# Kernel tuning notes

Measured on AMD Instinct MI355X. Metric: run time of the kernel, lower is better.

Reference implementation:

```python
import jax, jax.numpy as jnp
import numpy as np

STATE_MASS = 4.0
EPS = 1e-5
LOW_RANK_SCALE = 0.1  # _LOW_RANK_SCALE_INIT


def _ln(x, g, b):
    mu = jnp.mean(x, axis=-1, keepdims=True)
    var = jnp.var(x, axis=-1, keepdims=True)
    return (x - mu) * jax.lax.rsqrt(var + EPS) * g + b


def _signed_abs_softmax(s, axis=-1):
    s = jnp.nan_to_num(s)
    return jnp.sign(s) * jax.nn.softmax(jnp.abs(s), axis=axis)


def _signed_softmax_state(st):
    st = jnp.nan_to_num(st)
    return jnp.sign(st) * jax.nn.softmax(jnp.abs(st), axis=-1) * STATE_MASS


def _low_rank_scores(dst, src, Ut_w, Ut_b, Us_w, Us_b, w):
    # bilinear low-rank pairwise: score[b,i,j] = sum_r (dst_i Ut)_r * w_r * (src_j Us)_r
    pt = dst @ Ut_w + Ut_b                      # [B,Nd,R]
    ps = src @ Us_w + Us_b                      # [B,Ns,R]
    return jnp.einsum('bir,r,bjr->bij', pt, w * LOW_RANK_SCALE, ps)


def _gather_rows(x, idx):
    # x: [B,N,...], idx: [B,M,K] -> [B,M,K,...] (per-batch gather, no NxM broadcast)
    return jax.vmap(lambda xi, ii: xi[ii])(x, idx)


def setup_inputs() -> dict:
    key = jax.random.key(0)
    ks = jax.random.split(key, 8)
    B, S, D, M, R = 16, 2048, 512, 256, 64
    std = 0.02
    return {
        'token_val': jax.random.normal(ks[0], (B, S, D), jnp.float32),
        'token_state': jax.random.normal(ks[1], (B, S), jnp.float32),
        'init_state': jax.random.normal(ks[2], (M,), jnp.float32) * std,
        'init_val': jax.random.normal(ks[3], (M, D), jnp.float32) * std,
        'rUs_w': jax.random.normal(ks[4], (D, R), jnp.float32) * std,
        'rUs_b': jnp.zeros((R,), jnp.float32),
        'rUt_w': jax.random.normal(ks[5], (D, R), jnp.float32) * std,
        'rUt_b': jnp.zeros((R,), jnp.float32),
        'r_w': jnp.ones((R,), jnp.float32),
        'pUs_w': jax.random.normal(ks[6], (D, R), jnp.float32) * std,
        'pUs_b': jnp.zeros((R,), jnp.float32),
        'pUt_w': jax.random.normal(ks[7], (D, R), jnp.float32) * std,
        'pUt_b': jnp.zeros((R,), jnp.float32),
        'p_w': jnp.ones((R,), jnp.float32),
        'ln_g': jnp.ones((D,), jnp.float32),
        'ln_b': jnp.zeros((D,), jnp.float32),
        'topk': 16,
    }


def reference(token_val, token_state, init_state, init_val,
              rUs_w, rUs_b, rUt_w, rUt_b, r_w,
              pUs_w, pUs_b, pUt_w, pUt_b, p_w,
              ln_g, ln_b, topk):
    B = token_val.shape[0]
    M, D = init_val.shape

    # _MemoryLevel.initialize
    mem_state = _signed_softmax_state(jnp.broadcast_to(init_state, (B, M)))
    mem_val = _ln(jnp.broadcast_to(init_val, (B, M, D)), ln_g, ln_b)

    # ---- SparseTransition (write): route tokens -> slots, top-k sources/slot ----
    scores = _low_rank_scores(mem_val, token_val, rUt_w, rUt_b, rUs_w, rUs_b, r_w)  # [B,M,S]
    _, idx = jax.lax.top_k(jnp.abs(scores), topk)              # [B,M,K]
    sel = jnp.take_along_axis(scores, idx, axis=-1)            # [B,M,K]
    edges = _signed_abs_softmax(sel, axis=-1)                  # signed-abs-softmax over edges
    v_sel = _gather_rows(token_val, idx)                       # [B,M,K,D]
    s_sel = _gather_rows(token_state, idx)                     # [B,M,K]
    mem_val = mem_val + jnp.einsum('bmk,bmkd->bmd', edges, v_sel)   # merge_mode='add'
    mem_state = mem_state + jnp.einsum('bmk,bmk->bm', edges, s_sel)
    mem_state = _signed_softmax_state(mem_state)
    mem_val = _ln(mem_val, ln_g, ln_b)

    # ---- SparsePropagation within slots: state-weighted top-k edges, residual ----
    pscores = _low_rank_scores(mem_val, mem_val, pUt_w, pUt_b, pUs_w, pUs_b, p_w)   # [B,M,M]
    pscores = pscores * mem_state[:, None, :]                  # state_weight_edges
    _, pidx = jax.lax.top_k(jnp.abs(pscores), topk)            # [B,M,K]
    psel = jnp.take_along_axis(pscores, pidx, axis=-1)
    pe = _signed_abs_softmax(psel, axis=-1)
    pv = _gather_rows(mem_val, pidx)                           # [B,M,K,D]
    pst = _gather_rows(mem_state, pidx)                        # [B,M,K]
    mem_val = mem_val + jnp.einsum('bmk,bmkd->bmd', pe, pv)    # residual=True
    mem_state = mem_state + jnp.einsum('bmk,bmk->bm', pe, pst)
    mem_state = _signed_softmax_state(mem_state)
    mem_val = _ln(mem_val, ln_g, ln_b)
    return mem_val
```

## Files before the change

kernel.cpp:

```cpp
#include <hip/hip_runtime.h>
#include <hip/hip_bf16.h>
#include <math.h>

#define BB 16
#define SS 2048
#define DD 512
#define MM 256
#define RR 64
#define KK 16
#define GPAD 68

__device__ __forceinline__ float wave_sum(float v) {
#pragma unroll
  for (int off = 32; off > 0; off >>= 1) v += __shfl_xor(v, off);
  return v;
}

__device__ __forceinline__ float sgnf(float v) {
  return (v > 0.f) ? 1.f : ((v < 0.f) ? -1.f : 0.f);
}

__global__ __launch_bounds__(256) void k_init(
    const float* __restrict__ init_val, const float* __restrict__ init_state,
    const float* __restrict__ ln_g, const float* __restrict__ ln_b,
    const float* __restrict__ rUt_w, const float* __restrict__ rUt_b,
    const float* __restrict__ r_w, float* __restrict__ mv0,
    float* __restrict__ pt0, float* __restrict__ ms0) {
  int m = blockIdx.x, t = threadIdx.x;
  __shared__ float row[DD];
  __shared__ float red[8];
  __shared__ float red2[4];
  if (blockIdx.x == 0) {
    float v = init_state[t];
    float a = fabsf(v);
    float mx = a;
#pragma unroll
    for (int off = 32; off > 0; off >>= 1) mx = fmaxf(mx, __shfl_xor(mx, off));
    if ((t & 63) == 0) red2[t >> 6] = mx;
    __syncthreads();
    mx = fmaxf(fmaxf(red2[0], red2[1]), fmaxf(red2[2], red2[3]));
    __syncthreads();
    float e = expf(a - mx);
    float ssum = wave_sum(e);
    if ((t & 63) == 0) red2[t >> 6] = ssum;
    __syncthreads();
    ssum = red2[0] + red2[1] + red2[2] + red2[3];
    ms0[t] = sgnf(v) * e / ssum * 4.0f;
    __syncthreads();
  }
  float x0 = init_val[m * DD + t];
  float x1 = init_val[m * DD + t + 256];
  float s = wave_sum(x0 + x1);
  float sq = wave_sum(x0 * x0 + x1 * x1);
  if ((t & 63) == 0) { red[t >> 6] = s; red[4 + (t >> 6)] = sq; }
  __syncthreads();
  float mean = (red[0] + red[1] + red[2] + red[3]) * (1.0f / DD);
  float var = (red[4] + red[5] + red[6] + red[7]) * (1.0f / DD) - mean * mean;
  float rs = rsqrtf(var + 1e-5f);
  float n0 = (x0 - mean) * rs * ln_g[t] + ln_b[t];
  float n1 = (x1 - mean) * rs * ln_g[t + 256] + ln_b[t + 256];
  mv0[m * DD + t] = n0;
  mv0[m * DD + t + 256] = n1;
  row[t] = n0;
  row[t + 256] = n1;
  __syncthreads();
  if (t < RR) {
    float acc = rUt_b[t];
    for (int d = 0; d < DD; ++d) acc += row[d] * rUt_w[d * RR + t];
    pt0[m * RR + t] = acc * r_w[t] * 0.1f;
  }
}

__global__ __launch_bounds__(256) void k_state_softmax(
    const float* __restrict__ in, float* __restrict__ out) {
  int b = blockIdx.x, t = threadIdx.x;
  __shared__ float red[4];
  float v = in[b * MM + t];
  float a = fabsf(v);
  float mx = a;
#pragma unroll
  for (int off = 32; off > 0; off >>= 1) mx = fmaxf(mx, __shfl_xor(mx, off));
  if ((t & 63) == 0) red[t >> 6] = mx;
  __syncthreads();
  mx = fmaxf(fmaxf(red[0], red[1]), fmaxf(red[2], red[3]));
  __syncthreads();
  float e = expf(a - mx);
  float ssum = wave_sum(e);
  if ((t & 63) == 0) red[t >> 6] = ssum;
  __syncthreads();
  ssum = red[0] + red[1] + red[2] + red[3];
  out[b * MM + t] = sgnf(v) * e / ssum * 4.0f;
}

template <bool TRANS_OUT>
__device__ __forceinline__ void gemm_body(
    const float* __restrict__ A, const float* __restrict__ W,
    const float* __restrict__ bias, const float* __restrict__ colscale,
    float csmul, const float* __restrict__ rowscale, float* __restrict__ C,
    int row0, float (*Ast)[GPAD], float (*Ws)[GPAD]) {
  int tid = threadIdx.x;
  int ty = tid >> 4, tx = tid & 15;
  float acc[4][4] = {};
  for (int kc = 0; kc < DD; kc += 32) {
#pragma unroll
    for (int i = 0; i < 2; ++i) {
      int s4 = i * 256 + tid;
      int r = s4 >> 3;
      int k4 = s4 & 7;
      float4 v = *reinterpret_cast<const float4*>(
          &A[(size_t)(row0 + r) * DD + kc + k4 * 4]);
      Ast[k4 * 4 + 0][r] = v.x;
      Ast[k4 * 4 + 1][r] = v.y;
      Ast[k4 * 4 + 2][r] = v.z;
      Ast[k4 * 4 + 3][r] = v.w;
    }
#pragma unroll
    for (int i = 0; i < 2; ++i) {
      int s4 = i * 256 + tid;
      int r = s4 >> 4;
      int c4 = s4 & 15;
      float4 v = *reinterpret_cast<const float4*>(
          &W[(size_t)(kc + r) * RR + c4 * 4]);
      *reinterpret_cast<float4*>(&Ws[r][c4 * 4]) = v;
    }
    __syncthreads();
#pragma unroll
    for (int k = 0; k < 32; ++k) {
      float4 a4 = *reinterpret_cast<const float4*>(&Ast[k][ty * 4]);
      float4 w4 = *reinterpret_cast<const float4*>(&Ws[k][tx * 4]);
      acc[0][0] += a4.x * w4.x; acc[0][1] += a4.x * w4.y;
      acc[0][2] += a4.x * w4.z; acc[0][3] += a4.x * w4.w;
      acc[1][0] += a4.y * w4.x; acc[1][1] += a4.y * w4.y;
      acc[1][2] += a4.y * w4.z; acc[1][3] += a4.y * w4.w;
      acc[2][0] += a4.z * w4.x; acc[2][1] += a4.z * w4.y;
      acc[2][2] += a4.z * w4.z; acc[2][3] += a4.z * w4.w;
      acc[3][0] += a4.w * w4.x; acc[3][1] += a4.w * w4.y;
      acc[3][2] += a4.w * w4.z; acc[3][3] += a4.w * w4.w;
    }
    __syncthreads();
  }
#pragma unroll
  for (int i = 0; i < 4; ++i) {
    int rr = row0 + ty * 4 + i;
    float rsc = rowscale ? rowscale[rr] : 1.f;
    if (TRANS_OUT) {
#pragma unroll
      for (int j = 0; j < 4; ++j) {
        int cc = tx * 4 + j;
        float v = acc[i][j] + bias[cc];
        if (colscale) v *= colscale[cc] * csmul;
        v *= rsc;
        C[((size_t)(rr >> 8) * RR + cc) * MM + (rr & 255)] = v;
      }
    } else {
      float4 o;
      o.x = acc[i][0] + bias[tx * 4];
      o.y = acc[i][1] + bias[tx * 4 + 1];
      o.z = acc[i][2] + bias[tx * 4 + 2];
      o.w = acc[i][3] + bias[tx * 4 + 3];
      if (colscale) {
        o.x *= colscale[tx * 4] * csmul; o.y *= colscale[tx * 4 + 1] * csmul;
        o.z *= colscale[tx * 4 + 2] * csmul; o.w *= colscale[tx * 4 + 3] * csmul;
      }
      o.x *= rsc; o.y *= rsc; o.z *= rsc; o.w *= rsc;
      *reinterpret_cast<float4*>(&C[(size_t)rr * RR + tx * 4]) = o;
    }
  }
}

__global__ __launch_bounds__(256) void k_ps(
    const float* __restrict__ A, const float* __restrict__ W,
    const float* __restrict__ bias, float* __restrict__ C) {
  __shared__ float Ast[32][GPAD];
  __shared__ float Ws[32][GPAD];
  gemm_body<false>(A, W, bias, nullptr, 1.f, nullptr, C, blockIdx.x * 64,
                   Ast, Ws);
}

__global__ __launch_bounds__(256) void k_gemm_pair(
    const float* __restrict__ mv1, const float* __restrict__ pUt_w,
    const float* __restrict__ pUt_b, const float* __restrict__ p_w,
    const float* __restrict__ pUs_w, const float* __restrict__ pUs_b,
    const float* __restrict__ ms1, float* __restrict__ pt1,
    float* __restrict__ ps1T) {
  __shared__ float Ast[32][GPAD];
  __shared__ float Ws[32][GPAD];
  if (blockIdx.x < 64) {
    gemm_body<false>(mv1, pUt_w, pUt_b, p_w, 0.1f, nullptr, pt1,
                     blockIdx.x * 64, Ast, Ws);
  } else {
    gemm_body<true>(mv1, pUs_w, pUs_b, nullptr, 1.f, ms1, ps1T,
                    (blockIdx.x - 64) * 64, Ast, Ws);
  }
}

#define PSW 144
__device__ __forceinline__ int psw(int j) { return j + ((j >> 5) << 2); }

__global__ __launch_bounds__(256) void k_scores(
    const float* __restrict__ pt0, const float* __restrict__ ps,
    float* __restrict__ scores) {
  __shared__ float PtT[RR][128];
  __shared__ float PsT[RR][PSW];
  int t = threadIdx.x;
  int b = blockIdx.z;
  int m0 = blockIdx.y * 128;
  int j0 = blockIdx.x * 128;
#pragma unroll
  for (int ii = 0; ii < 2; ++ii) {
    int slot = ii * 256 + t;
    int tm4 = slot >> 4, tk4 = slot & 15;
    const float* base = pt0 + (size_t)(m0 + tm4 * 4) * RR + tk4 * 4;
    float4 v0 = *reinterpret_cast<const float4*>(base);
    float4 v1 = *reinterpret_cast<const float4*>(base + RR);
    float4 v2 = *reinterpret_cast<const float4*>(base + 2 * RR);
    float4 v3 = *reinterpret_cast<const float4*>(base + 3 * RR);
    float4 w;
    w.x = v0.x; w.y = v1.x; w.z = v2.x; w.w = v3.x;
    *reinterpret_cast<float4*>(&PtT[tk4 * 4 + 0][tm4 * 4]) = w;
    w.x = v0.y; w.y = v1.y; w.z = v2.y; w.w = v3.y;
    *reinterpret_cast<float4*>(&PtT[tk4 * 4 + 1][tm4 * 4]) = w;
    w.x = v0.z; w.y = v1.z; w.z = v2.z; w.w = v3.z;
    *reinterpret_cast<float4*>(&PtT[tk4 * 4 + 2][tm4 * 4]) = w;
    w.x = v0.w; w.y = v1.w; w.z = v2.w; w.w = v3.w;
    *reinterpret_cast<float4*>(&PtT[tk4 * 4 + 3][tm4 * 4]) = w;
  }
#pragma unroll
  for (int ii = 0; ii < 2; ++ii) {
    int slot = ii * 256 + t;
    int jt = slot >> 4, kt = slot & 15;
    const float* base = ps + ((size_t)b * SS + j0 + jt * 4) * RR + kt * 4;
    float4 v0 = *reinterpret_cast<const float4*>(base);
    float4 v1 = *reinterpret_cast<const float4*>(base + RR);
    float4 v2 = *reinterpret_cast<const float4*>(base + 2 * RR);
    float4 v3 = *reinterpret_cast<const float4*>(base + 3 * RR);
    int jc = psw(jt * 4);
    float4 w;
    w.x = v0.x; w.y = v1.x; w.z = v2.x; w.w = v3.x;
    *reinterpret_cast<float4*>(&PsT[kt * 4 + 0][jc]) = w;
    w.x = v0.y; w.y = v1.y; w.z = v2.y; w.w = v3.y;
    *reinterpret_cast<float4*>(&PsT[kt * 4 + 1][jc]) = w;
    w.x = v0.z; w.y = v1.z; w.z = v2.z; w.w = v3.z;
    *reinterpret_cast<float4*>(&PsT[kt * 4 + 2][jc]) = w;
    w.x = v0.w; w.y = v1.w; w.z = v2.w; w.w = v3.w;
    *reinterpret_cast<float4*>(&PsT[kt * 4 + 3][jc]) = w;
  }
  __syncthreads();
  int jg = t & 15;
  int mg = t >> 4;
  int jlo = psw(jg * 8);
  float acc[8][8] = {};
#pragma unroll
  for (int k = 0; k < RR; ++k) {
    float4 a0 = *reinterpret_cast<const float4*>(&PtT[k][mg * 8]);
    float4 a1 = *reinterpret_cast<const float4*>(&PtT[k][mg * 8 + 4]);
    float4 w0 = *reinterpret_cast<const float4*>(&PsT[k][jlo]);
    float4 w1 = *reinterpret_cast<const float4*>(&PsT[k][jlo + 4]);
    float av[8] = {a0.x, a0.y, a0.z, a0.w, a1.x, a1.y, a1.z, a1.w};
    float wv[8] = {w0.x, w0.y, w0.z, w0.w, w1.x, w1.y, w1.z, w1.w};
#pragma unroll
    for (int r = 0; r < 8; ++r)
#pragma unroll
      for (int cc = 0; cc < 8; ++cc) acc[r][cc] += av[r] * wv[cc];
  }
  float* obase =
      scores + (size_t)b * MM * SS + (size_t)(m0 + mg * 8) * SS + j0 + jg * 8;
#pragma unroll
  for (int r = 0; r < 8; ++r) {
    float4 o0, o1;
    o0.x = acc[r][0]; o0.y = acc[r][1]; o0.z = acc[r][2]; o0.w = acc[r][3];
    o1.x = acc[r][4]; o1.y = acc[r][5]; o1.z = acc[r][6]; o1.w = acc[r][7];
    *reinterpret_cast<float4*>(obase + (size_t)r * SS) = o0;
    *reinterpret_cast<float4*>(obase + (size_t)r * SS + 4) = o1;
  }
}

__global__ __launch_bounds__(256) void k_write(
    const float* __restrict__ scores, const float* __restrict__ token_val,
    const float* __restrict__ token_state, const float* __restrict__ mv0,
    const float* __restrict__ ms0, const float* __restrict__ ln_g,
    const float* __restrict__ ln_b, float* __restrict__ mv1,
    float* __restrict__ ms_w) {
  int t = threadIdx.x;
  int wave = t >> 6, lane = t & 63;
  int i = blockIdx.x;
  int slot = i >> 3;
  int b = 2 * (i & 7) + (slot >> 6);
  int m = (slot & 63) * 4 + wave;
  int row = b * MM + m;
  __shared__ int selj_sh[4][KK];
  const float* srow = scores + (size_t)row * SS;
  unsigned au[32];
  unsigned maxa = 0u;
#pragma unroll
  for (int ch = 0; ch < 8; ++ch) {
    float4 q = *reinterpret_cast<const float4*>(srow + (ch * 64 + lane) * 4);
    au[ch * 4 + 0] = __float_as_uint(q.x) & 0x7fffffffu;
    au[ch * 4 + 1] = __float_as_uint(q.y) & 0x7fffffffu;
    au[ch * 4 + 2] = __float_as_uint(q.z) & 0x7fffffffu;
    au[ch * 4 + 3] = __float_as_uint(q.w) & 0x7fffffffu;
    maxa = max(maxa, max(max(au[ch * 4], au[ch * 4 + 1]),
                         max(au[ch * 4 + 2], au[ch * 4 + 3])));
  }
#pragma unroll
  for (int off = 32; off > 0; off >>= 1)
    maxa = max(maxa, (unsigned)__shfl_xor((int)maxa, off));
  unsigned lo = 0u, hi = maxa, thr = 0u;
  bool early = false;
  while (lo < hi) {
    unsigned mid = lo + ((hi - lo + 1u) >> 1);
    int cnt = 0;
#pragma unroll
    for (int c = 0; c < 32; ++c) cnt += __popcll(__ballot(au[c] >= mid));
    if (cnt == KK) { thr = mid; early = true; break; }
    if (cnt > KK) lo = mid; else hi = mid - 1u;
  }
  if (!early) thr = lo;
  unsigned long long ltmask = (1ull << lane) - 1ull;
  int s = 0;
  unsigned tiemask = 0u;
#pragma unroll
  for (int c = 0; c < 32; ++c) {
    bool sg = early ? (au[c] >= thr) : (au[c] > thr);
    unsigned long long mk = __ballot(sg);
    if (sg)
      selj_sh[wave][s + __popcll(mk & ltmask)] =
          (c >> 2) * 256 + lane * 4 + (c & 3);
    s += __popcll(mk);
    if (!early && au[c] == thr) tiemask |= 1u << c;
  }
  int taken = s;
  while (taken < KK) {
    int myj = 0x7fffffff;
#pragma unroll
    for (int c = 0; c < 32; ++c)
      if ((tiemask >> c) & 1u) {
        int j = (c >> 2) * 256 + lane * 4 + (c & 3);
        myj = min(myj, j);
      }
    int wj = myj;
#pragma unroll
    for (int off = 32; off > 0; off >>= 1) wj = min(wj, __shfl_xor(wj, off));
    if (wj == 0x7fffffff) break;
    if (((wj >> 2) & 63) == lane) tiemask &= ~(1u << (((wj >> 8) << 2) | (wj & 3)));
    if (lane == 0) selj_sh[wave][taken] = wj;
    ++taken;
  }
  int js[KK];
  float es[KK];
#pragma unroll
  for (int k = 0; k < KK; ++k) {
    js[k] = selj_sh[wave][k];
    es[k] = srow[js[k]];
  }
  float mx = 0.f;
#pragma unroll
  for (int k = 0; k < KK; ++k) mx = fmaxf(mx, fabsf(es[k]));
  float ssum = 0.f;
#pragma unroll
  for (int k = 0; k < KK; ++k) {
    float ex = expf(fabsf(es[k]) - mx);
    ssum += ex;
    es[k] = sgnf(es[k]) * ex;
  }
  float inv = 1.f / ssum;
  int dbase = lane * 8;
  const float* m0row = mv0 + m * DD + dbase;
  float4 a0 = *reinterpret_cast<const float4*>(m0row);
  float4 a1 = *reinterpret_cast<const float4*>(m0row + 4);
  float acc[8] = {a0.x, a0.y, a0.z, a0.w, a1.x, a1.y, a1.z, a1.w};
  float stacc = 0.f;
#pragma unroll
  for (int k = 0; k < KK; ++k) {
    float e = es[k] * inv;
    const float* tv = token_val + ((size_t)b * SS + js[k]) * DD + dbase;
    float4 u0 = *reinterpret_cast<const float4*>(tv);
    float4 u1 = *reinterpret_cast<const float4*>(tv + 4);
    acc[0] += e * u0.x; acc[1] += e * u0.y; acc[2] += e * u0.z; acc[3] += e * u0.w;
    acc[4] += e * u1.x; acc[5] += e * u1.y; acc[6] += e * u1.z; acc[7] += e * u1.w;
    stacc += e * token_state[(size_t)b * SS + js[k]];
  }
  if (lane == 0) ms_w[row] = ms0[m] + stacc;
  float s1 = 0.f, s2 = 0.f;
#pragma unroll
  for (int c = 0; c < 8; ++c) { s1 += acc[c]; s2 += acc[c] * acc[c]; }
  s1 = wave_sum(s1);
  s2 = wave_sum(s2);
  float mean = s1 * (1.0f / DD);
  float var = s2 * (1.0f / DD) - mean * mean;
  float rs = rsqrtf(var + 1e-5f);
  float4 g0 = *reinterpret_cast<const float4*>(ln_g + dbase);
  float4 g1 = *reinterpret_cast<const float4*>(ln_g + dbase + 4);
  float4 b0v = *reinterpret_cast<const float4*>(ln_b + dbase);
  float4 b1v = *reinterpret_cast<const float4*>(ln_b + dbase + 4);
  float4 o0, o1;
  o0.x = (acc[0] - mean) * rs * g0.x + b0v.x;
  o0.y = (acc[1] - mean) * rs * g0.y + b0v.y;
  o0.z = (acc[2] - mean) * rs * g0.z + b0v.z;
  o0.w = (acc[3] - mean) * rs * g0.w + b0v.w;
  o1.x = (acc[4] - mean) * rs * g1.x + b1v.x;
  o1.y = (acc[5] - mean) * rs * g1.y + b1v.y;
  o1.z = (acc[6] - mean) * rs * g1.z + b1v.z;
  o1.w = (acc[7] - mean) * rs * g1.w + b1v.w;
  float* orow = mv1 + (size_t)row * DD + dbase;
  *reinterpret_cast<float4*>(orow) = o0;
  *reinterpret_cast<float4*>(orow + 4) = o1;
}

__global__ __launch_bounds__(256, 4) void k_prop(
    const float* __restrict__ pt1, const float* __restrict__ ps1T,
    const float* __restrict__ mv1, const float* __restrict__ ln_g,
    const float* __restrict__ ln_b, float* __restrict__ out) {
  int t = threadIdx.x;
  int wave = t >> 6, lane = t & 63;
  int row = blockIdx.x * 4 + wave;
  int b = row >> 8, m = row & 255;
  __shared__ int selj_sh[4][KK];
  __shared__ float selv_sh[4][KK];
  float ptval = pt1[(size_t)row * RR + lane];
  const float* pB = ps1T + (size_t)b * RR * MM + lane * 4;
  float sc[4] = {0.f, 0.f, 0.f, 0.f};
#pragma unroll 8
  for (int r = 0; r < RR; ++r) {
    float w = __shfl(ptval, r);
    float4 pv = *reinterpret_cast<const float4*>(pB + r * MM);
    sc[0] += w * pv.x; sc[1] += w * pv.y; sc[2] += w * pv.z; sc[3] += w * pv.w;
  }
  int jbase = lane * 4;
  unsigned au[4];
#pragma unroll
  for (int c = 0; c < 4; ++c) au[c] = __float_as_uint(sc[c]) & 0x7fffffffu;
  unsigned lo = 0u, hi = 0x7f800000u, thr = 0u;
  bool early = false;
  while (lo < hi) {
    unsigned mid = lo + ((hi - lo + 1u) >> 1);
    int cnt = 0;
#pragma unroll
    for (int c = 0; c < 4; ++c) cnt += __popcll(__ballot(au[c] >= mid));
    if (cnt == KK) { thr = mid; early = true; break; }
    if (cnt > KK) lo = mid; else hi = mid - 1u;
  }
  if (!early) thr = lo;
  unsigned long long ltmask = (1ull << lane) - 1ull;
  int s = 0;
  unsigned tiemask = 0u;
#pragma unroll
  for (int c = 0; c < 4; ++c) {
    bool sg = early ? (au[c] >= thr) : (au[c] > thr);
    unsigned long long mk = __ballot(sg);
    if (sg) {
      int slot = s + __popcll(mk & ltmask);
      selj_sh[wave][slot] = jbase + c;
      selv_sh[wave][slot] = sc[c];
    }
    s += __popcll(mk);
    if (!early && au[c] == thr) tiemask |= 1u << c;
  }
  int taken = s;
  while (taken < KK) {
    int myj = 0x7fffffff;
#pragma unroll
    for (int c = 0; c < 4; ++c)
      if ((tiemask >> c) & 1u) myj = min(myj, jbase + c);
    int wj = myj;
#pragma unroll
    for (int off = 32; off > 0; off >>= 1) wj = min(wj, __shfl_xor(wj, off));
    if (wj == 0x7fffffff) break;
    if (wj >= jbase && wj < jbase + 4) {
      tiemask &= ~(1u << (wj - jbase));
      selv_sh[wave][taken] = sc[wj - jbase];
      if (lane == (wj >> 2)) selj_sh[wave][taken] = wj;
    }
    ++taken;
  }
  int js[KK];
  float es[KK];
#pragma unroll
  for (int k = 0; k < KK; ++k) { js[k] = selj_sh[wave][k]; es[k] = selv_sh[wave][k]; }
  float mx = 0.f;
#pragma unroll
  for (int k = 0; k < KK; ++k) mx = fmaxf(mx, fabsf(es[k]));
  float ssum = 0.f;
#pragma unroll
  for (int k = 0; k < KK; ++k) {
    float ex = expf(fabsf(es[k]) - mx);
    ssum += ex;
    es[k] = sgnf(es[k]) * ex;
  }
  float inv = 1.f / ssum;
  int dbase = lane * 8;
  const float* mrow = mv1 + (size_t)row * DD + dbase;
  float4 a0 = *reinterpret_cast<const float4*>(mrow);
  float4 a1 = *reinterpret_cast<const float4*>(mrow + 4);
  float acc[8] = {a0.x, a0.y, a0.z, a0.w, a1.x, a1.y, a1.z, a1.w};
#pragma unroll
  for (int k = 0; k < KK; ++k) {
    float e = es[k] * inv;
    const float* pv = mv1 + ((size_t)b * MM + js[k]) * DD + dbase;
    float4 u0 = *reinterpret_cast<const float4*>(pv);
    float4 u1 = *reinterpret_cast<const float4*>(pv + 4);
    acc[0] += e * u0.x; acc[1] += e * u0.y; acc[2] += e * u0.z; acc[3] += e * u0.w;
    acc[4] += e * u1.x; acc[5] += e * u1.y; acc[6] += e * u1.z; acc[7] += e * u1.w;
  }
  float s1 = 0.f, s2 = 0.f;
#pragma unroll
  for (int c = 0; c < 8; ++c) { s1 += acc[c]; s2 += acc[c] * acc[c]; }
  s1 = wave_sum(s1);
  s2 = wave_sum(s2);
  float mean = s1 * (1.0f / DD);
  float var = s2 * (1.0f / DD) - mean * mean;
  float rs = rsqrtf(var + 1e-5f);
  float4 g0 = *reinterpret_cast<const float4*>(ln_g + dbase);
  float4 g1 = *reinterpret_cast<const float4*>(ln_g + dbase + 4);
  float4 b0v = *reinterpret_cast<const float4*>(ln_b + dbase);
  float4 b1v = *reinterpret_cast<const float4*>(ln_b + dbase + 4);
  float4 o0, o1;
  o0.x = (acc[0] - mean) * rs * g0.x + b0v.x;
  o0.y = (acc[1] - mean) * rs * g0.y + b0v.y;
  o0.z = (acc[2] - mean) * rs * g0.z + b0v.z;
  o0.w = (acc[3] - mean) * rs * g0.w + b0v.w;
  o1.x = (acc[4] - mean) * rs * g1.x + b1v.x;
  o1.y = (acc[5] - mean) * rs * g1.y + b1v.y;
  o1.z = (acc[6] - mean) * rs * g1.z + b1v.z;
  o1.w = (acc[7] - mean) * rs * g1.w + b1v.w;
  float* orow = out + (size_t)row * DD + dbase;
  *reinterpret_cast<float4*>(orow) = o0;
  *reinterpret_cast<float4*>(orow + 4) = o1;
}

extern "C" void kernel_launch(void* const* d_in, const int* in_sizes, int n_in,
                              void* d_out, int out_size, void* d_ws,
                              size_t ws_size, hipStream_t stream) {
  const float* token_val = (const float*)d_in[0];
  const float* token_state = (const float*)d_in[1];
  const float* init_state = (const float*)d_in[2];
  const float* init_val = (const float*)d_in[3];
  const float* rUs_w = (const float*)d_in[4];
  const float* rUs_b = (const float*)d_in[5];
  const float* rUt_w = (const float*)d_in[6];
  const float* rUt_b = (const float*)d_in[7];
  const float* r_w = (const float*)d_in[8];
  const float* pUs_w = (const float*)d_in[9];
  const float* pUs_b = (const float*)d_in[10];
  const float* pUt_w = (const float*)d_in[11];
  const float* pUt_b = (const float*)d_in[12];
  const float* p_w = (const float*)d_in[13];
  const float* ln_g = (const float*)d_in[14];
  const float* ln_b = (const float*)d_in[15];
  float* out = (float*)d_out;

  float* ws = (float*)d_ws;
  float* mv0 = ws;    ws += MM * DD;
  float* pt0 = ws;    ws += MM * RR;
  float* ms0 = ws;    ws += MM;
  float* ps = ws;     ws += (size_t)BB * SS * RR;
  float* scores = ws; ws += (size_t)BB * MM * SS;
  float* mv1 = ws;    ws += (size_t)BB * MM * DD;
  float* ms_w = ws;   ws += BB * MM;
  float* ms1 = ws;    ws += BB * MM;
  float* pt1 = ws;    ws += (size_t)BB * MM * RR;
  float* ps1T = ws;   ws += (size_t)BB * RR * MM;

  k_init<<<MM, 256, 0, stream>>>(init_val, init_state, ln_g, ln_b, rUt_w,
                                 rUt_b, r_w, mv0, pt0, ms0);
  k_ps<<<(BB * SS) / 64, 256, 0, stream>>>(token_val, rUs_w, rUs_b, ps);
  dim3 gs(SS / 128, MM / 128, BB);
  k_scores<<<gs, 256, 0, stream>>>(pt0, ps, scores);
  k_write<<<(BB * MM) / 4, 256, 0, stream>>>(scores, token_val, token_state,
                                             mv0, ms0, ln_g, ln_b, mv1, ms_w);
  k_state_softmax<<<BB, 256, 0, stream>>>(ms_w, ms1);
  k_gemm_pair<<<128, 256, 0, stream>>>(mv1, pUt_w, pUt_b, p_w, pUs_w, pUs_b,
                                       ms1, pt1, ps1T);
  k_prop<<<(BB * MM) / 4, 256, 0, stream>>>(pt1, ps1T, mv1, ln_g, ln_b, out);
}
```

Baseline: 159.2 us.

## Fuse init into ps GEMM launch and state softmax into propagation kernel

Merges the init kernel (memory layernorm, initial state softmax, pt0 projection) into the token projection GEMM launch as extra blocks, so both run concurrently in one dispatch. The separate state-softmax kernel is removed: each k_prop block recomputes the per-batch signed softmax into shared memory and applies the state weighting to scores there, rather than folding it into ps1T in the GEMM epilogue. The init projection is also split across all four waves with a shared-memory partial reduction. Together these cut two kernel launches and some serialization, at the cost of redundant per-block softmax work in k_prop.

```diff
diff --git a/kernel.cpp b/kernel.cpp
--- a/kernel.cpp
+++ b/kernel.cpp
@@ -20,31 +20,114 @@
   return (v > 0.f) ? 1.f : ((v < 0.f) ? -1.f : 0.f);
 }
 
-__global__ __launch_bounds__(256) void k_init(
+template <bool TRANS_OUT>
+__device__ __forceinline__ void gemm_body(
+    const float* __restrict__ A, const float* __restrict__ W,
+    const float* __restrict__ bias, const float* __restrict__ colscale,
+    float csmul, float* __restrict__ C, int row0, float (*Ast)[GPAD],
+    float (*Ws)[GPAD]) {
+  int tid = threadIdx.x;
+  int ty = tid >> 4, tx = tid & 15;
+  float acc[4][4] = {};
+  for (int kc = 0; kc < DD; kc += 32) {
+#pragma unroll
+    for (int i = 0; i < 2; ++i) {
+      int s4 = i * 256 + tid;
+      int r = s4 >> 3;
+      int k4 = s4 & 7;
+      float4 v = *reinterpret_cast<const float4*>(
+          &A[(size_t)(row0 + r) * DD + kc + k4 * 4]);
+      Ast[k4 * 4 + 0][r] = v.x;
+      Ast[k4 * 4 + 1][r] = v.y;
+      Ast[k4 * 4 + 2][r] = v.z;
+      Ast[k4 * 4 + 3][r] = v.w;
+    }
+#pragma unroll
+    for (int i = 0; i < 2; ++i) {
+      int s4 = i * 256 + tid;
+      int r = s4 >> 4;
+      int c4 = s4 & 15;
+      float4 v = *reinterpret_cast<const float4*>(
+          &W[(size_t)(kc + r) * RR + c4 * 4]);
+      *reinterpret_cast<float4*>(&Ws[r][c4 * 4]) = v;
+    }
+    __syncthreads();
+#pragma unroll
+    for (int k = 0; k < 32; ++k) {
+      float4 a4 = *reinterpret_cast<const float4*>(&Ast[k][ty * 4]);
+      float4 w4 = *reinterpret_cast<const float4*>(&Ws[k][tx * 4]);
+      acc[0][0] += a4.x * w4.x; acc[0][1] += a4.x * w4.y;
+      acc[0][2] += a4.x * w4.z; acc[0][3] += a4.x * w4.w;
+      acc[1][0] += a4.y * w4.x; acc[1][1] += a4.y * w4.y;
+      acc[1][2] += a4.y * w4.z; acc[1][3] += a4.y * w4.w;
+      acc[2][0] += a4.z * w4.x; acc[2][1] += a4.z * w4.y;
+      acc[2][2] += a4.z * w4.z; acc[2][3] += a4.z * w4.w;
+      acc[3][0] += a4.w * w4.x; acc[3][1] += a4.w * w4.y;
+      acc[3][2] += a4.w * w4.z; acc[3][3] += a4.w * w4.w;
+    }
+    __syncthreads();
+  }
+#pragma unroll
+  for (int i = 0; i < 4; ++i) {
+    int rr = row0 + ty * 4 + i;
+    if (TRANS_OUT) {
+#pragma unroll
+      for (int j = 0; j < 4; ++j) {
+        int cc = tx * 4 + j;
+        float v = acc[i][j] + bias[cc];
+        if (colscale) v *= colscale[cc] * csmul;
+        C[((size_t)(rr >> 8) * RR + cc) * MM + (rr & 255)] = v;
+      }
+    } else {
+      float4 o;
+      o.x = acc[i][0] + bias[tx * 4];
+      o.y = acc[i][1] + bias[tx * 4 + 1];
+      o.z = acc[i][2] + bias[tx * 4 + 2];
+      o.w = acc[i][3] + bias[tx * 4 + 3];
+      if (colscale) {
+        o.x *= colscale[tx * 4] * csmul; o.y *= colscale[tx * 4 + 1] * csmul;
+        o.z *= colscale[tx * 4 + 2] * csmul; o.w *= colscale[tx * 4 + 3] * csmul;
+      }
+      *reinterpret_cast<float4*>(&C[(size_t)rr * RR + tx * 4]) = o;
+    }
+  }
+}
+
+__global__ __launch_bounds__(256) void k_ps_init(
+    const float* __restrict__ token_val, const float* __restrict__ rUs_w,
+    const float* __restrict__ rUs_b, float* __restrict__ ps,
     const float* __restrict__ init_val, const float* __restrict__ init_state,
     const float* __restrict__ ln_g, const float* __restrict__ ln_b,
     const float* __restrict__ rUt_w, const float* __restrict__ rUt_b,
     const float* __restrict__ r_w, float* __restrict__ mv0,
     float* __restrict__ pt0, float* __restrict__ ms0) {
-  int m = blockIdx.x, t = threadIdx.x;
-  __shared__ float row[DD];
-  __shared__ float red[8];
-  __shared__ float red2[4];
-  if (blockIdx.x == 0) {
+  __shared__ float Ast[32][GPAD];
+  __shared__ float Ws[32][GPAD];
+  int t = threadIdx.x;
+  if (blockIdx.x < 512) {
+    gemm_body<false>(token_val, rUs_w, rUs_b, nullptr, 1.f, ps,
+                     blockIdx.x * 64, Ast, Ws);
+    return;
+  }
+  int m = blockIdx.x - 512;
+  float* row = &Ast[0][0];
+  float* red = &Ws[0][0];
+  float* part = &Ws[1][0];
+  if (m == 0) {
     float v = init_state[t];
     float a = fabsf(v);
     float mx = a;
 #pragma unroll
     for (int off = 32; off > 0; off >>= 1) mx = fmaxf(mx, __shfl_xor(mx, off));
-    if ((t & 63) == 0) red2[t >> 6] = mx;
-    __syncthreads();
-    mx = fmaxf(fmaxf(red2[0], red2[1]), fmaxf(red2[2], red2[3]));
+    if ((t & 63) == 0) red[4 + (t >> 6)] = mx;
+    __syncthreads();
+    mx = fmaxf(fmaxf(red[4], red[5]), fmaxf(red[6], red[7]));
     __syncthreads();
     float e = expf(a - mx);
     float ssum = wave_sum(e);
-    if ((t & 63) == 0) red2[t >> 6] = ssum;
-    __syncthreads();
-    ssum = red2[0] + red2[1] + red2[2] + red2[3];
+    if ((t & 63) == 0) red[4 + (t >> 6)] = ssum;
+    __syncthreads();
+    ssum = red[4] + red[5] + red[6] + red[7];
     ms0[t] = sgnf(v) * e / ssum * 4.0f;
     __syncthreads();
   }
@@ -52,6 +135,7 @@
   float x1 = init_val[m * DD + t + 256];
   float s = wave_sum(x0 + x1);
   float sq = wave_sum(x0 * x0 + x1 * x1);
+  __syncthreads();
   if ((t & 63) == 0) { red[t >> 6] = s; red[4 + (t >> 6)] = sq; }
   __syncthreads();
   float mean = (red[0] + red[1] + red[2] + red[3]) * (1.0f / DD);
@@ -64,132 +148,34 @@
   row[t] = n0;
   row[t + 256] = n1;
   __syncthreads();
+  {
+    int r = t & 63, q = t >> 6;
+    float acc = 0.f;
+    const float* wp = rUt_w + (size_t)(q * 128) * RR + r;
+#pragma unroll 16
+    for (int d = 0; d < 128; ++d) acc += row[q * 128 + d] * wp[d * RR];
+    part[q * RR + r] = acc;
+  }
+  __syncthreads();
   if (t < RR) {
-    float acc = rUt_b[t];
-    for (int d = 0; d < DD; ++d) acc += row[d] * rUt_w[d * RR + t];
+    float acc = part[t] + part[RR + t] + part[2 * RR + t] + part[3 * RR + t] +
+                rUt_b[t];
     pt0[m * RR + t] = acc * r_w[t] * 0.1f;
   }
-}
-
-__global__ __launch_bounds__(256) void k_state_softmax(
-    const float* __restrict__ in, float* __restrict__ out) {
-  int b = blockIdx.x, t = threadIdx.x;
-  __shared__ float red[4];
-  float v = in[b * MM + t];
-  float a = fabsf(v);
-  float mx = a;
-#pragma unroll
-  for (int off = 32; off > 0; off >>= 1) mx = fmaxf(mx, __shfl_xor(mx, off));
-  if ((t & 63) == 0) red[t >> 6] = mx;
-  __syncthreads();
-  mx = fmaxf(fmaxf(red[0], red[1]), fmaxf(red[2], red[3]));
-  __syncthreads();
-  float e = expf(a - mx);
-  float ssum = wave_sum(e);
-  if ((t & 63) == 0) red[t >> 6] = ssum;
-  __syncthreads();
-  ssum = red[0] + red[1] + red[2] + red[3];
-  out[b * MM + t] = sgnf(v) * e / ssum * 4.0f;
-}
-
-template <bool TRANS_OUT>
-__device__ __forceinline__ void gemm_body(
-    const float* __restrict__ A, const float* __restrict__ W,
-    const float* __restrict__ bias, const float* __restrict__ colscale,
-    float csmul, const float* __restrict__ rowscale, float* __restrict__ C,
-    int row0, float (*Ast)[GPAD], float (*Ws)[GPAD]) {
-  int tid = threadIdx.x;
-  int ty = tid >> 4, tx = tid & 15;
-  float acc[4][4] = {};
-  for (int kc = 0; kc < DD; kc += 32) {
-#pragma unroll
-    for (int i = 0; i < 2; ++i) {
-      int s4 = i * 256 + tid;
-      int r = s4 >> 3;
-      int k4 = s4 & 7;
-      float4 v = *reinterpret_cast<const float4*>(
-          &A[(size_t)(row0 + r) * DD + kc + k4 * 4]);
-      Ast[k4 * 4 + 0][r] = v.x;
-      Ast[k4 * 4 + 1][r] = v.y;
-      Ast[k4 * 4 + 2][r] = v.z;
-      Ast[k4 * 4 + 3][r] = v.w;
-    }
-#pragma unroll
-    for (int i = 0; i < 2; ++i) {
-      int s4 = i * 256 + tid;
-      int r = s4 >> 4;
-      int c4 = s4 & 15;
-      float4 v = *reinterpret_cast<const float4*>(
-          &W[(size_t)(kc + r) * RR + c4 * 4]);
-      *reinterpret_cast<float4*>(&Ws[r][c4 * 4]) = v;
-    }
-    __syncthreads();
-#pragma unroll
-    for (int k = 0; k < 32; ++k) {
-      float4 a4 = *reinterpret_cast<const float4*>(&Ast[k][ty * 4]);
-      float4 w4 = *reinterpret_cast<const float4*>(&Ws[k][tx * 4]);
-      acc[0][0] += a4.x * w4.x; acc[0][1] += a4.x * w4.y;
-      acc[0][2] += a4.x * w4.z; acc[0][3] += a4.x * w4.w;
-      acc[1][0] += a4.y * w4.x; acc[1][1] += a4.y * w4.y;
-      acc[1][2] += a4.y * w4.z; acc[1][3] += a4.y * w4.w;
-      acc[2][0] += a4.z * w4.x; acc[2][1] += a4.z * w4.y;
-      acc[2][2] += a4.z * w4.z; acc[2][3] += a4.z * w4.w;
-      acc[3][0] += a4.w * w4.x; acc[3][1] += a4.w * w4.y;
-      acc[3][2] += a4.w * w4.z; acc[3][3] += a4.w * w4.w;
-    }
-    __syncthreads();
-  }
-#pragma unroll
-  for (int i = 0; i < 4; ++i) {
-    int rr = row0 + ty * 4 + i;
-    float rsc = rowscale ? rowscale[rr] : 1.f;
-    if (TRANS_OUT) {
-#pragma unroll
-      for (int j = 0; j < 4; ++j) {
-        int cc = tx * 4 + j;
-        float v = acc[i][j] + bias[cc];
-        if (colscale) v *= colscale[cc] * csmul;
-        v *= rsc;
-        C[((size_t)(rr >> 8) * RR + cc) * MM + (rr & 255)] = v;
-      }
-    } else {
-      float4 o;
-      o.x = acc[i][0] + bias[tx * 4];
-      o.y = acc[i][1] + bias[tx * 4 + 1];
-      o.z = acc[i][2] + bias[tx * 4 + 2];
-      o.w = acc[i][3] + bias[tx * 4 + 3];
-      if (colscale) {
-        o.x *= colscale[tx * 4] * csmul; o.y *= colscale[tx * 4 + 1] * csmul;
-        o.z *= colscale[tx * 4 + 2] * csmul; o.w *= colscale[tx * 4 + 3] * csmul;
-      }
-      o.x *= rsc; o.y *= rsc; o.z *= rsc; o.w *= rsc;
-      *reinterpret_cast<float4*>(&C[(size_t)rr * RR + tx * 4]) = o;
-    }
-  }
-}
-
-__global__ __launch_bounds__(256) void k_ps(
-    const float* __restrict__ A, const float* __restrict__ W,
-    const float* __restrict__ bias, float* __restrict__ C) {
-  __shared__ float Ast[32][GPAD];
-  __shared__ float Ws[32][GPAD];
-  gemm_body<false>(A, W, bias, nullptr, 1.f, nullptr, C, blockIdx.x * 64,
-                   Ast, Ws);
 }
 
 __global__ __launch_bounds__(256) void k_gemm_pair(
     const float* __restrict__ mv1, const float* __restrict__ pUt_w,
     const float* __restrict__ pUt_b, const float* __restrict__ p_w,
     const float* __restrict__ pUs_w, const float* __restrict__ pUs_b,
-    const float* __restrict__ ms1, float* __restrict__ pt1,
-    float* __restrict__ ps1T) {
+    float* __restrict__ pt1, float* __restrict__ ps1T) {
   __shared__ float Ast[32][GPAD];
   __shared__ float Ws[32][GPAD];
   if (blockIdx.x < 64) {
-    gemm_body<false>(mv1, pUt_w, pUt_b, p_w, 0.1f, nullptr, pt1,
-                     blockIdx.x * 64, Ast, Ws);
+    gemm_body<false>(mv1, pUt_w, pUt_b, p_w, 0.1f, pt1, blockIdx.x * 64,
+                     Ast, Ws);
   } else {
-    gemm_body<true>(mv1, pUs_w, pUs_b, nullptr, 1.f, ms1, ps1T,
+    gemm_body<true>(mv1, pUs_w, pUs_b, nullptr, 1.f, ps1T,
                     (blockIdx.x - 64) * 64, Ast, Ws);
   }
 }
@@ -409,14 +395,35 @@
 
 __global__ __launch_bounds__(256, 4) void k_prop(
     const float* __restrict__ pt1, const float* __restrict__ ps1T,
-    const float* __restrict__ mv1, const float* __restrict__ ln_g,
-    const float* __restrict__ ln_b, float* __restrict__ out) {
+    const float* __restrict__ ms_w, const float* __restrict__ mv1,
+    const float* __restrict__ ln_g, const float* __restrict__ ln_b,
+    float* __restrict__ out) {
   int t = threadIdx.x;
   int wave = t >> 6, lane = t & 63;
   int row = blockIdx.x * 4 + wave;
   int b = row >> 8, m = row & 255;
   __shared__ int selj_sh[4][KK];
   __shared__ float selv_sh[4][KK];
+  __shared__ float ms1_sh[MM];
+  __shared__ float red[4];
+  {
+    float v = ms_w[b * MM + t];
+    float a = fabsf(v);
+    float mx = a;
+#pragma unroll
+    for (int off = 32; off > 0; off >>= 1) mx = fmaxf(mx, __shfl_xor(mx, off));
+    if ((t & 63) == 0) red[t >> 6] = mx;
+    __syncthreads();
+    mx = fmaxf(fmaxf(red[0], red[1]), fmaxf(red[2], red[3]));
+    __syncthreads();
+    float e = expf(a - mx);
+    float ssum = wave_sum(e);
+    if ((t & 63) == 0) red[t >> 6] = ssum;
+    __syncthreads();
+    ssum = red[0] + red[1] + red[2] + red[3];
+    ms1_sh[t] = sgnf(v) * e / ssum * 4.0f;
+  }
+  __syncthreads();
   float ptval = pt1[(size_t)row * RR + lane];
   const float* pB = ps1T + (size_t)b * RR * MM + lane * 4;
   float sc[4] = {0.f, 0.f, 0.f, 0.f};
@@ -427,6 +434,8 @@
     sc[0] += w * pv.x; sc[1] += w * pv.y; sc[2] += w * pv.z; sc[3] += w * pv.w;
   }
   int jbase = lane * 4;
+#pragma unroll
+  for (int c = 0; c < 4; ++c) sc[c] *= ms1_sh[jbase + c];
   unsigned au[4];
 #pragma unroll
   for (int c = 0; c < 4; ++c) au[c] = __float_as_uint(sc[c]) & 0x7fffffffu;
@@ -557,19 +566,18 @@
   float* scores = ws; ws += (size_t)BB * MM * SS;
   float* mv1 = ws;    ws += (size_t)BB * MM * DD;
   float* ms_w = ws;   ws += BB * MM;
-  float* ms1 = ws;    ws += BB * MM;
   float* pt1 = ws;    ws += (size_t)BB * MM * RR;
   float* ps1T = ws;   ws += (size_t)BB * RR * MM;
 
-  k_init<<<MM, 256, 0, stream>>>(init_val, init_state, ln_g, ln_b, rUt_w,
-                                 rUt_b, r_w, mv0, pt0, ms0);
-  k_ps<<<(BB * SS) / 64, 256, 0, stream>>>(token_val, rUs_w, rUs_b, ps);
+  k_ps_init<<<768, 256, 0, stream>>>(token_val, rUs_w, rUs_b, ps, init_val,
+                                     init_state, ln_g, ln_b, rUt_w, rUt_b,
+                                     r_w, mv0, pt0, ms0);
   dim3 gs(SS / 128, MM / 128, BB);
   k_scores<<<gs, 256, 0, stream>>>(pt0, ps, scores);
   k_write<<<(BB * MM) / 4, 256, 0, stream>>>(scores, token_val, token_state,
                                              mv0, ms0, ln_g, ln_b, mv1, ms_w);
-  k_state_softmax<<<BB, 256, 0, stream>>>(ms_w, ms1);
   k_gemm_pair<<<128, 256, 0, stream>>>(mv1, pUt_w, pUt_b, p_w, pUs_w, pUs_b,
-                                       ms1, pt1, ps1T);
-  k_prop<<<(BB * MM) / 4, 256, 0, stream>>>(pt1, ps1T, mv1, ln_g, ln_b, out);
-}
+                                       pt1, ps1T);
+  k_prop<<<(BB * MM) / 4, 256, 0, stream>>>(pt1, ps1T, ms_w, mv1, ln_g, ln_b,
+                                            out);
+}
```

After: 148.3 us, median of 2. 6.9% less time.
